# Performance work log

Measured on AMD Instinct MI355X. Metric: run time of the kernel, lower is better.

## Reference

```python
import jax, jax.numpy as jnp
import numpy as np

N_ENT = 14541
EMB_DIM = 768
TOP_K = 1000
NEG_TIMES = 5
BS = 128
MARGIN = 0.5


def setup_inputs() -> dict:
    key = jax.random.key(0)
    ks = jax.random.split(key, 12)
    return {
        "pos_stelp_score": jax.random.uniform(ks[0], (BS,), dtype=jnp.float32),
        "pos_rotate_score": jax.random.uniform(ks[1], (BS,), dtype=jnp.float32),
        "ent_idx": jax.random.randint(ks[2], (BS, TOP_K), 0, N_ENT),
        "neg_stelp_scores": jax.random.uniform(ks[3], (BS, NEG_TIMES), dtype=jnp.float32),
        "neg_rotate_scores": jax.random.uniform(ks[4], (BS, NEG_TIMES), dtype=jnp.float32),
        "stelp_scores": jax.random.uniform(ks[5], (BS, TOP_K), dtype=jnp.float32),
        "rotate_scores": jax.random.uniform(ks[6], (BS, TOP_K), dtype=jnp.float32),
        "stelp_ent_emb": jax.random.normal(ks[7], (N_ENT, EMB_DIM), dtype=jnp.float32),
        "simi_score_mtx": jax.random.normal(ks[8], (N_ENT, N_ENT), dtype=jnp.float32),
        "proj_w": jax.random.normal(ks[9], (1, 5 * TOP_K + EMB_DIM), dtype=jnp.float32) * 0.02,
        "proj_b": jnp.zeros((1,), dtype=jnp.float32),
    }


def reference(pos_stelp_score, pos_rotate_score, ent_idx, neg_stelp_scores,
              neg_rotate_scores, stelp_scores, rotate_scores,
              stelp_ent_emb, simi_score_mtx, proj_w, proj_b):
    # get_alpha: per-sample gather of embedding rows + similarity rows
    emb = stelp_ent_emb[ent_idx]                       # [bs, top_k, emb_dim]
    emb_std = jnp.std(emb, axis=1, ddof=1)             # torch.std is unbiased -> [bs, emb_dim]
    # torch: gather rows of simi_score_mtx then mean over last dim.
    # Equivalent (and avoids a [bs, top_k, n_ent] intermediate): mean rows first, then gather.
    simi_row_mean = jnp.mean(simi_score_mtx, axis=-1)  # [n_ent]
    simi = simi_row_mean[ent_idx]                      # [bs, top_k]
    score_sub = jnp.abs(rotate_scores - stelp_scores)
    score_add = stelp_scores + rotate_scores
    feature = jnp.concatenate(
        [emb_std, simi, score_sub, score_add, stelp_scores, rotate_scores], axis=1)
    alpha = jax.nn.sigmoid(feature @ proj_w.T + proj_b)[:, 0]  # [bs]

    pos_ens = alpha * pos_stelp_score + (1.0 - alpha) * pos_rotate_score          # [bs]
    neg_ens = alpha[:, None] * neg_stelp_scores + (1.0 - alpha)[:, None] * neg_rotate_scores
    loss = jnp.mean(jax.nn.relu(MARGIN - pos_ens[:, None] + neg_ens))
    return loss
```

## Files before the change

kernel.cpp:

```cpp
#include <hip/hip_runtime.h>
#include <math.h>
#include <stdint.h>

#define N_ENT 14541
#define EMB_DIM 768
#define TOP_K 1000
#define NEG_TIMES 5
#define BS 128
#define MARGIN 0.5f
#define KCHUNKS 4
#define KPER (TOP_K / KCHUNKS)

#define MEAN_OFF 0
#define PART_OFF 16384
#define LOSS_OFF (PART_OFF + BS * KCHUNKS * 2 * EMB_DIM)

__device__ __forceinline__ float blockReduceSum(float v) {
    __shared__ float red[16];
    int lane = threadIdx.x & 63;
    int wid  = threadIdx.x >> 6;
#pragma unroll
    for (int o = 32; o > 0; o >>= 1) v += __shfl_down(v, o, 64);
    __syncthreads();
    if (lane == 0) red[wid] = v;
    __syncthreads();
    float s = 0.f;
    if (threadIdx.x == 0) {
        int nw = (blockDim.x + 63) >> 6;
        s = red[0];
        for (int i = 1; i < nw; ++i) s += red[i];
    }
    return s;
}

__global__ void row_mean_kernel(const float* __restrict__ simi,
                                float* __restrict__ mean) {
    int row = blockIdx.x;
    const float* p = simi + (size_t)row * N_ENT;
    float s = 0.f;

    uintptr_t addr = (uintptr_t)p;
    int head = (int)(((16u - (addr & 15u)) & 15u) >> 2);
    if (head > N_ENT) head = N_ENT;
    if ((int)threadIdx.x < head) s += p[threadIdx.x];

    int n = N_ENT - head;
    const float4* p4 = (const float4*)(p + head);
    int n4 = n >> 2;
    for (int i = threadIdx.x; i < n4; i += 256) {
        float4 v = p4[i];
        s += (v.x + v.y) + (v.z + v.w);
    }
    int tail = n & 3;
    if ((int)threadIdx.x < tail) s += p[head + (n4 << 2) + threadIdx.x];

    s = blockReduceSum(s);
    if (threadIdx.x == 0) mean[row] = s * (1.0f / N_ENT);
}

__global__ void emb_partial_kernel(const int* __restrict__ ent_idx,
                                   const float* __restrict__ emb,
                                   float* __restrict__ part) {
    int b = blockIdx.x >> 2;
    int c = blockIdx.x & 3;
    int t = threadIdx.x;

    __shared__ int sidx[KPER];
    const int* idx = ent_idx + b * TOP_K + c * KPER;
    for (int k = t; k < KPER; k += 256) sidx[k] = idx[k];
    __syncthreads();

    float s1a = 0.f, s1b = 0.f, s1c = 0.f;
    float s2a = 0.f, s2b = 0.f, s2c = 0.f;
#pragma unroll 4
    for (int k = 0; k < KPER; ++k) {
        const float* r = emb + (size_t)sidx[k] * EMB_DIM;
        float a = r[t];
        float bb = r[t + 256];
        float cc = r[t + 512];
        s1a += a;  s2a += a * a;
        s1b += bb; s2b += bb * bb;
        s1c += cc; s2c += cc * cc;
    }

    float* o = part + (size_t)blockIdx.x * (2 * EMB_DIM);
    o[t]           = s1a; o[t + 256]           = s1b; o[t + 512]           = s1c;
    o[EMB_DIM + t] = s2a; o[EMB_DIM + 256 + t] = s2b; o[EMB_DIM + 512 + t] = s2c;
}

__global__ void finalize_kernel(const float* __restrict__ mean,
                                const float* __restrict__ part,
                                const int* __restrict__ ent_idx,
                                const float* __restrict__ stelp,
                                const float* __restrict__ rotate,
                                const float* __restrict__ w,
                                const float* __restrict__ bbias,
                                const float* __restrict__ pos_s,
                                const float* __restrict__ pos_r,
                                const float* __restrict__ neg_s,
                                const float* __restrict__ neg_r,
                                float* __restrict__ loss_part) {
    int b = blockIdx.x;
    int t = threadIdx.x;
    float acc = 0.f;

    const float* pb = part + (size_t)b * KCHUNKS * 2 * EMB_DIM;
#pragma unroll
    for (int j = 0; j < 3; ++j) {
        int d = t + j * 256;
        float s1 = pb[d] + pb[1536 + d] + pb[3072 + d] + pb[4608 + d];
        float s2 = pb[EMB_DIM + d] + pb[1536 + EMB_DIM + d] +
                   pb[3072 + EMB_DIM + d] + pb[4608 + EMB_DIM + d];
        float var = (s2 - s1 * s1 * (1.0f / TOP_K)) * (1.0f / (TOP_K - 1));
        var = fmaxf(var, 0.f);
        acc += sqrtf(var) * w[d];
    }

    for (int k = t; k < TOP_K; k += 256) {
        int e = ent_idx[b * TOP_K + k];
        float sm = mean[e];
        float s = stelp[b * TOP_K + k];
        float r = rotate[b * TOP_K + k];
        acc += sm * w[EMB_DIM + k]
             + fabsf(r - s) * w[EMB_DIM + TOP_K + k]
             + (s + r) * w[EMB_DIM + 2 * TOP_K + k]
             + s * w[EMB_DIM + 3 * TOP_K + k]
             + r * w[EMB_DIM + 4 * TOP_K + k];
    }

    float logit = blockReduceSum(acc);
    if (t == 0) {
        logit += bbias[0];
        float alpha = 1.0f / (1.0f + expf(-logit));
        float pe = alpha * pos_s[b] + (1.0f - alpha) * pos_r[b];
        float l = 0.f;
#pragma unroll
        for (int j = 0; j < NEG_TIMES; ++j) {
            float ne = alpha * neg_s[b * NEG_TIMES + j] +
                       (1.0f - alpha) * neg_r[b * NEG_TIMES + j];
            l += fmaxf(0.f, MARGIN - pe + ne);
        }
        loss_part[b] = l;
    }
}

__global__ void reduce_loss_kernel(const float* __restrict__ loss_part,
                                   float* __restrict__ out) {
    float v = ((int)threadIdx.x < BS) ? loss_part[threadIdx.x] : 0.f;
    v = blockReduceSum(v);
    if (threadIdx.x == 0) out[0] = v * (1.0f / (BS * NEG_TIMES));
}

extern "C" void kernel_launch(void* const* d_in, const int* in_sizes, int n_in,
                              void* d_out, int out_size, void* d_ws, size_t ws_size,
                              hipStream_t stream) {
    const float* pos_s  = (const float*)d_in[0];
    const float* pos_r  = (const float*)d_in[1];
    const int*   ent_i  = (const int*)d_in[2];
    const float* neg_s  = (const float*)d_in[3];
    const float* neg_r  = (const float*)d_in[4];
    const float* stelp  = (const float*)d_in[5];
    const float* rotate = (const float*)d_in[6];
    const float* emb    = (const float*)d_in[7];
    const float* simi   = (const float*)d_in[8];
    const float* w      = (const float*)d_in[9];
    const float* bb     = (const float*)d_in[10];

    float* ws    = (float*)d_ws;
    float* mean  = ws + MEAN_OFF;
    float* part  = ws + PART_OFF;
    float* lossp = ws + LOSS_OFF;
    float* out   = (float*)d_out;

    hipLaunchKernelGGL(row_mean_kernel, dim3(N_ENT), dim3(256), 0, stream, simi, mean);
    hipLaunchKernelGGL(emb_partial_kernel, dim3(BS * KCHUNKS), dim3(256), 0, stream,
                       ent_i, emb, part);
    hipLaunchKernelGGL(finalize_kernel, dim3(BS), dim3(256), 0, stream,
                       mean, part, ent_i, stelp, rotate, w, bb,
                       pos_s, pos_r, neg_s, neg_r, lossp);
    hipLaunchKernelGGL(reduce_loss_kernel, dim3(1), dim3(128), 0, stream, lossp, out);
}
```

Before: 1.140 ms.

## Merge row-mean and embedding-stats kernels into one grid, doubling K chunks

Combines the similarity row-mean kernel and the embedding gather/statistics kernel into a single launch, with the embedding blocks placed first in the grid so their latency-bound gathers overlap the bandwidth-bound streaming of the 846MB similarity matrix. The number of K chunks per batch row goes from 4 to 8, giving 1024 gather blocks, and the finalize kernel loops over chunks generically. This saves a launch and a serialization point, at the cost of more partial sums to reduce.

Result: faster. 1.115 ms (-2.2%).

```diff
diff --git a/kernel.cpp b/kernel.cpp
--- a/kernel.cpp
+++ b/kernel.cpp
@@ -8,8 +8,9 @@
 #define NEG_TIMES 5
 #define BS 128
 #define MARGIN 0.5f
-#define KCHUNKS 4
+#define KCHUNKS 8
 #define KPER (TOP_K / KCHUNKS)
+#define EMB_BLOCKS (BS * KCHUNKS)
 
 #define MEAN_OFF 0
 #define PART_OFF 16384
@@ -33,59 +34,61 @@
     return s;
 }
 
-__global__ void row_mean_kernel(const float* __restrict__ simi,
-                                float* __restrict__ mean) {
-    int row = blockIdx.x;
-    const float* p = simi + (size_t)row * N_ENT;
-    float s = 0.f;
+__global__ void stage1_kernel(const float* __restrict__ simi,
+                              float* __restrict__ mean,
+                              const int* __restrict__ ent_idx,
+                              const float* __restrict__ emb,
+                              float* __restrict__ part) {
+    if (blockIdx.x < EMB_BLOCKS) {
+        int blk = blockIdx.x;
+        int b = blk >> 3;
+        int c = blk & 7;
+        int t = threadIdx.x;
 
-    uintptr_t addr = (uintptr_t)p;
-    int head = (int)(((16u - (addr & 15u)) & 15u) >> 2);
-    if (head > N_ENT) head = N_ENT;
-    if ((int)threadIdx.x < head) s += p[threadIdx.x];
+        __shared__ int sidx[KPER];
+        const int* idx = ent_idx + b * TOP_K + c * KPER;
+        if (t < KPER) sidx[t] = idx[t];
+        __syncthreads();
 
-    int n = N_ENT - head;
-    const float4* p4 = (const float4*)(p + head);
-    int n4 = n >> 2;
-    for (int i = threadIdx.x; i < n4; i += 256) {
-        float4 v = p4[i];
-        s += (v.x + v.y) + (v.z + v.w);
+        float s1a = 0.f, s1b = 0.f, s1c = 0.f;
+        float s2a = 0.f, s2b = 0.f, s2c = 0.f;
+#pragma unroll 5
+        for (int k = 0; k < KPER; ++k) {
+            const float* r = emb + (size_t)sidx[k] * EMB_DIM;
+            float a  = r[t];
+            float bb = r[t + 256];
+            float cc = r[t + 512];
+            s1a += a;  s2a += a * a;
+            s1b += bb; s2b += bb * bb;
+            s1c += cc; s2c += cc * cc;
+        }
+
+        float* o = part + (size_t)blk * (2 * EMB_DIM);
+        o[t]           = s1a; o[t + 256]           = s1b; o[t + 512]           = s1c;
+        o[EMB_DIM + t] = s2a; o[EMB_DIM + 256 + t] = s2b; o[EMB_DIM + 512 + t] = s2c;
+    } else {
+        int row = blockIdx.x - EMB_BLOCKS;
+        const float* p = simi + (size_t)row * N_ENT;
+        float s = 0.f;
+
+        uintptr_t addr = (uintptr_t)p;
+        int head = (int)(((16u - (addr & 15u)) & 15u) >> 2);
+        if (head > N_ENT) head = N_ENT;
+        if ((int)threadIdx.x < head) s += p[threadIdx.x];
+
+        int n = N_ENT - head;
+        const float4* p4 = (const float4*)(p + head);
+        int n4 = n >> 2;
+        for (int i = threadIdx.x; i < n4; i += 256) {
+            float4 v = p4[i];
+            s += (v.x + v.y) + (v.z + v.w);
+        }
+        int tail = n & 3;
+        if ((int)threadIdx.x < tail) s += p[head + (n4 << 2) + threadIdx.x];
+
+        s = blockReduceSum(s);
+        if (threadIdx.x == 0) mean[row] = s * (1.0f / N_ENT);
     }
-    int tail = n & 3;
-    if ((int)threadIdx.x < tail) s += p[head + (n4 << 2) + threadIdx.x];
-
-    s = blockReduceSum(s);
-    if (threadIdx.x == 0) mean[row] = s * (1.0f / N_ENT);
-}
-
-__global__ void emb_partial_kernel(const int* __restrict__ ent_idx,
-                                   const float* __restrict__ emb,
-                                   float* __restrict__ part) {
-    int b = blockIdx.x >> 2;
-    int c = blockIdx.x & 3;
-    int t = threadIdx.x;
-
-    __shared__ int sidx[KPER];
-    const int* idx = ent_idx + b * TOP_K + c * KPER;
-    for (int k = t; k < KPER; k += 256) sidx[k] = idx[k];
-    __syncthreads();
-
-    float s1a = 0.f, s1b = 0.f, s1c = 0.f;
-    float s2a = 0.f, s2b = 0.f, s2c = 0.f;
-#pragma unroll 4
-    for (int k = 0; k < KPER; ++k) {
-        const float* r = emb + (size_t)sidx[k] * EMB_DIM;
-        float a = r[t];
-        float bb = r[t + 256];
-        float cc = r[t + 512];
-        s1a += a;  s2a += a * a;
-        s1b += bb; s2b += bb * bb;
-        s1c += cc; s2c += cc * cc;
-    }
-
-    float* o = part + (size_t)blockIdx.x * (2 * EMB_DIM);
-    o[t]           = s1a; o[t + 256]           = s1b; o[t + 512]           = s1c;
-    o[EMB_DIM + t] = s2a; o[EMB_DIM + 256 + t] = s2b; o[EMB_DIM + 512 + t] = s2c;
 }
 
 __global__ void finalize_kernel(const float* __restrict__ mean,
@@ -108,9 +111,12 @@
 #pragma unroll
     for (int j = 0; j < 3; ++j) {
         int d = t + j * 256;
-        float s1 = pb[d] + pb[1536 + d] + pb[3072 + d] + pb[4608 + d];
-        float s2 = pb[EMB_DIM + d] + pb[1536 + EMB_DIM + d] +
-                   pb[3072 + EMB_DIM + d] + pb[4608 + EMB_DIM + d];
+        float s1 = 0.f, s2 = 0.f;
+#pragma unroll
+        for (int c = 0; c < KCHUNKS; ++c) {
+            s1 += pb[c * (2 * EMB_DIM) + d];
+            s2 += pb[c * (2 * EMB_DIM) + EMB_DIM + d];
+        }
         float var = (s2 - s1 * s1 * (1.0f / TOP_K)) * (1.0f / (TOP_K - 1));
         var = fmaxf(var, 0.f);
         acc += sqrtf(var) * w[d];
@@ -172,9 +178,8 @@
     float* lossp = ws + LOSS_OFF;
     float* out   = (float*)d_out;
 
-    hipLaunchKernelGGL(row_mean_kernel, dim3(N_ENT), dim3(256), 0, stream, simi, mean);
-    hipLaunchKernelGGL(emb_partial_kernel, dim3(BS * KCHUNKS), dim3(256), 0, stream,
-                       ent_i, emb, part);
+    hipLaunchKernelGGL(stage1_kernel, dim3(EMB_BLOCKS + N_ENT), dim3(256), 0, stream,
+                       simi, mean, ent_i, emb, part);
     hipLaunchKernelGGL(finalize_kernel, dim3(BS), dim3(256), 0, stream,
                        mean, part, ent_i, stelp, rotate, w, bb,
                        pos_s, pos_r, neg_s, neg_r, lossp);
```
